# Optimization experiments

Measured on AMD Instinct MI355X. Metric: run time of the kernel, lower is better.

## Reference

```python
import jax, jax.numpy as jnp
import numpy as np

SOS = 1
H = 1024   # hidden_size
V = 32000  # vocab_size
B = 64     # batch
S = 50     # encoder (source) length
T = 25     # decode steps (target length)


def setup_inputs() -> dict:
    key = jax.random.key(0)
    ks = jax.random.split(key, 16)
    s = 1.0 / np.sqrt(H)

    def u(k, shape):
        return jax.random.uniform(k, shape, jnp.float32, -s, s)

    return {
        "encoder_outputs": jax.random.normal(ks[0], (B, S, H), jnp.float32),
        "encoder_hidden": jax.random.normal(ks[1], (1, B, H), jnp.float32),
        "target_tensor": jax.random.randint(ks[2], (B, T), 0, V),
        "emb": jax.random.normal(ks[3], (V, H), jnp.float32),       # nn.Embedding
        "Wa": u(ks[4], (H, H)), "ba": u(ks[5], (H,)),               # attention query proj
        "Ua": u(ks[6], (H, H)), "bu": u(ks[7], (H,)),               # attention key proj
        "Va": u(ks[8], (H, 1)), "bv": u(ks[9], (1,)),               # attention score vector
        "W_ih": u(ks[10], (3 * H, 2 * H)), "b_ih": u(ks[11], (3 * H,)),  # GRU input weights
        "W_hh": u(ks[12], (3 * H, H)), "b_hh": u(ks[13], (3 * H,)),     # GRU hidden weights
        "Wout": u(ks[14], (V, H)), "bout": u(ks[15], (V,)),         # output linear
    }


def reference(encoder_outputs, encoder_hidden, target_tensor, emb,
              Wa, ba, Ua, bu, Va, bv, W_ih, b_ih, W_hh, b_hh, Wout, bout):
    # Bahdanau key projection is independent of the decode step: precompute once.
    keys_proj = encoder_outputs @ Ua.T + bu        # [B, S, H]
    h0 = encoder_hidden[0]                         # [B, H]

    # Teacher forcing: input at step i is SOS then target[:, :-1]. (Dropout in eval mode = identity.)
    sos = jnp.full((B, 1), SOS, dtype=target_tensor.dtype)
    tokens = jnp.concatenate([sos, target_tensor[:, :-1]], axis=1).T  # [T, B]

    def step(h, tok):
        x_emb = emb[tok]                                         # [B, H]
        q = h @ Wa.T + ba                                        # [B, H] (query = hidden)
        scores = jnp.tanh(q[:, None, :] + keys_proj) @ Va        # [B, S, 1]
        w = jax.nn.softmax(scores[..., 0] + bv[0], axis=-1)      # [B, S]
        context = jnp.einsum('bs,bsh->bh', w, encoder_outputs)   # [B, H]
        x = jnp.concatenate([x_emb, context], axis=-1)           # [B, 2H]
        gx = x @ W_ih.T + b_ih                                   # [B, 3H]
        gh = h @ W_hh.T + b_hh                                   # [B, 3H]
        rx, zx, nx = jnp.split(gx, 3, axis=-1)                   # PyTorch gate order r,z,n
        rh, zh, nh = jnp.split(gh, 3, axis=-1)
        r = jax.nn.sigmoid(rx + rh)
        z = jax.nn.sigmoid(zx + zh)
        n = jnp.tanh(nx + r * nh)
        h_new = (1.0 - z) * n + z * h
        logits = h_new @ Wout.T + bout                           # [B, V]
        return h_new, logits

    _, logits = jax.lax.scan(step, h0, tokens)                   # [T, B, V]
    return jnp.transpose(logits, (1, 0, 2))                      # [B, T, V]
```

## Files before the change

kernel.cpp:

```cpp
#include <hip/hip_runtime.h>
#include <hip/hip_bf16.h>

#define BB_ 64
#define SS_ 50
#define TT_ 25
#define HH_ 1024
#define VV_ 32000

typedef __bf16 bf16x8 __attribute__((ext_vector_type(8)));
typedef float f32x4 __attribute__((ext_vector_type(4)));
typedef unsigned long long u64;

__device__ __forceinline__ unsigned short f2b(float f) {
  unsigned u = __float_as_uint(f);
  u = (u + 0x7FFFu + ((u >> 16) & 1u)) >> 16;
  return (unsigned short)u;
}
__device__ __forceinline__ float b2f_(unsigned short s) {
  return __uint_as_float((unsigned)s << 16);
}
__device__ __forceinline__ float fast_tanh(float x) {
  float e = __expf(2.f * x);
  return 1.f - 2.f / (e + 1.f);
}
__device__ __forceinline__ float fast_sigmoid(float x) {
  return 1.f / (1.f + __expf(-x));
}
__device__ __forceinline__ void gload16(const void* g, void* l) {
  __builtin_amdgcn_global_load_lds((const __attribute__((address_space(1))) void*)g,
                                   (__attribute__((address_space(3))) void*)l, 16, 0, 0);
}
__device__ __forceinline__ bf16x8 ldb8(const unsigned short* p) {
  return *(const bf16x8*)p;
}

__device__ __forceinline__ void cstf(float* p, float v) {
  __hip_atomic_store(p, v, __ATOMIC_RELAXED, __HIP_MEMORY_SCOPE_AGENT);
}
__device__ __forceinline__ void cst4(unsigned* p, unsigned v) {
  __hip_atomic_store(p, v, __ATOMIC_RELAXED, __HIP_MEMORY_SCOPE_AGENT);
}
__device__ __forceinline__ unsigned cadd(unsigned* p) {
  return __hip_atomic_fetch_add(p, 1u, __ATOMIC_RELAXED, __HIP_MEMORY_SCOPE_AGENT);
}
__device__ __forceinline__ unsigned cldu(const unsigned* p) {
  return __hip_atomic_load(p, __ATOMIC_RELAXED, __HIP_MEMORY_SCOPE_AGENT);
}

#define F_QR   0
#define F_GHR  128
#define F_CTXR 256
#define F_HR   384
#define F_MINI 512

__global__ __launch_bounds__(256) void cvt_bf16(const float* __restrict__ src,
                                                unsigned short* __restrict__ dst, long n) {
  long i = ((long)blockIdx.x * 256 + threadIdx.x) * 4;
  if (i >= n) return;
  float4 v = *(const float4*)(src + i);
  *(ushort4*)(dst + i) = make_ushort4(f2b(v.x), f2b(v.y), f2b(v.z), f2b(v.w));
}

__global__ __launch_bounds__(256) void embed_gather(const int* __restrict__ tgt,
                                                    const float* __restrict__ emb,
                                                    unsigned short* __restrict__ X) {
  long idx = ((long)blockIdx.x * 256 + threadIdx.x) * 4;
  if (idx >= (long)1600 * HH_) return;
  int col = (int)(idx & (HH_ - 1));
  int r = (int)(idx >> 10);
  int t = r % 25;
  int tok = (t == 0) ? 1 : tgt[r - 1];
  float4 v = *(const float4*)(emb + (long)tok * HH_ + col);
  *(ushort4*)(X + idx) = make_ushort4(f2b(v.x), f2b(v.y), f2b(v.z), f2b(v.w));
}

__global__ __launch_bounds__(256) void init_h(const float* __restrict__ eh,
                                              unsigned short* __restrict__ HBROT,
                                              unsigned* __restrict__ cnt) {
  if (blockIdx.x == 0) {
    for (int k = threadIdx.x; k < 4096; k += 256) cnt[k] = 0;
  }
  int i = (blockIdx.x * 256 + threadIdx.x) * 4;
  if (i >= BB_ * HH_) return;
  float4 v = *(const float4*)(eh + i);
  *(ushort4*)(HBROT + i) = make_ushort4(f2b(v.x), f2b(v.y), f2b(v.z), f2b(v.w));
}

__global__ __launch_bounds__(256) void gemm128_bt(
    const unsigned short* __restrict__ A, const unsigned short* __restrict__ W,
    const float* __restrict__ bias, float* __restrict__ out, long ldo,
    int Mtiles, int ldw, int Mvalid) {
  __shared__ __align__(16) unsigned short As[128 * 32];
  __shared__ __align__(16) unsigned short Bs[128 * 32];
  int nwg = gridDim.x;
  int orig = blockIdx.x;
  int xcd = orig & 7, lid = orig >> 3;
  int qq = nwg >> 3, rr = nwg & 7;
  int wgid = (xcd < rr ? xcd * (qq + 1) : rr * (qq + 1) + (xcd - rr) * qq) + lid;
  int m0 = (wgid % Mtiles) * 128;
  int n0 = (wgid / Mtiles) * 128;
  int tid = threadIdx.x;
  int w = tid >> 6, l = tid & 63;
  int srow = tid >> 2, scg = tid & 3;
  int mw = (w & 1) * 64, nw = (w >> 1) * 64;

  const unsigned short* Ag0 = A + (long)(m0 + srow) * 1024 + scg * 8;
  const unsigned short* Ag1 = Ag0 + 64 * 1024;
  const unsigned short* Wg0 = W + (long)(n0 + srow) * ldw + scg * 8;
  const unsigned short* Wg1 = Wg0 + (long)64 * ldw;
  unsigned short* lA0 = As + tid * 8;
  unsigned short* lA1 = As + 2048 + tid * 8;
  unsigned short* lB0 = Bs + tid * 8;
  unsigned short* lB1 = Bs + 2048 + tid * 8;

  f32x4 zero = {0.f, 0.f, 0.f, 0.f};
  f32x4 acc[4][4];
#pragma unroll
  for (int i = 0; i < 4; ++i)
#pragma unroll
    for (int j = 0; j < 4; ++j) acc[i][j] = zero;

  for (int k0 = 0; k0 < 1024; k0 += 32) {
    __syncthreads();
    gload16(Ag0 + k0, lA0);
    gload16(Ag1 + k0, lA1);
    gload16(Wg0 + k0, lB0);
    gload16(Wg1 + k0, lB1);
    __syncthreads();
    bf16x8 af[4], bg[4];
#pragma unroll
    for (int mt = 0; mt < 4; ++mt)
      af[mt] = ldb8(As + (mw + mt * 16 + (l & 15)) * 32 + (l >> 4) * 8);
#pragma unroll
    for (int nt = 0; nt < 4; ++nt)
      bg[nt] = ldb8(Bs + (nw + nt * 16 + (l & 15)) * 32 + (l >> 4) * 8);
#pragma unroll
    for (int mt = 0; mt < 4; ++mt)
#pragma unroll
      for (int nt = 0; nt < 4; ++nt)
        acc[mt][nt] = __builtin_amdgcn_mfma_f32_16x16x32_bf16(af[mt], bg[nt], acc[mt][nt], 0, 0, 0);
  }

  int lr = (l >> 4) * 4, lc = l & 15;
#pragma unroll
  for (int nt = 0; nt < 4; ++nt) {
    int col = n0 + nw + nt * 16 + lc;
    float bv = bias[col];
#pragma unroll
    for (int mt = 0; mt < 4; ++mt) {
#pragma unroll
      for (int r = 0; r < 4; ++r) {
        int m = m0 + mw + mt * 16 + lr + r;
        if (m < Mvalid) out[(long)m * ldo + col] = acc[mt][nt][r] + bv;
      }
    }
  }
}

__global__ __launch_bounds__(256) void decode_loop(
    const unsigned short* __restrict__ WaB, const unsigned short* __restrict__ WhhB,
    const unsigned short* __restrict__ WihB, const float* __restrict__ ba,
    const float* __restrict__ bhh, const float* __restrict__ Va,
    const unsigned short* __restrict__ KEYSB, const unsigned short* __restrict__ ENCB,
    const float* __restrict__ GA, const float* __restrict__ ehid,
    float* __restrict__ QROT, float* __restrict__ GHROT, float* __restrict__ SCROT,
    unsigned short* __restrict__ CTXROT, unsigned short* __restrict__ HBROT,
    unsigned short* __restrict__ HALLB, unsigned* __restrict__ cnt) {
  __shared__ __align__(16) char AsC[16 * 2048];
  __shared__ float qs[1024];
  __shared__ float vas[1024];
  __shared__ float wgt[64];

  const int tid = threadIdx.x, bid = blockIdx.x;
  const int wv = tid >> 6, l = tid & 63;
  const int lc = l & 15, hi = l >> 4, ko = hi * 8, lr4 = hi * 4;
  const int xcd = bid & 7, lxb = bid >> 3;
  const int mt_ = lxb & 3, cg = lxb >> 2;
  const int qcls = xcd >> 1;

  const int m1 = mt_ * 16;
  const int nch = xcd * 32 + cg * 4 + wv;
  const int n1 = nch * 16;
  const bool isq = (n1 < 1024);
  const unsigned short* B1 = isq ? WaB + (long)(n1 + lc) * 1024 + ko
                                 : WhhB + (long)(n1 - 1024 + lc) * 1024 + ko;
  float* o1 = isq ? QROT + n1 : GHROT + (n1 - 1024);
  const long ldo1 = isq ? 1024 : 3072;
  const long slot1 = isq ? (long)BB_ * 1024 : (long)BB_ * 3072;
  const float bv1 = isq ? ba[n1 + lc] : bhh[n1 - 1024 + lc];

  const int b2 = xcd * 8 + cg;
  const int jq = mt_ * 4 + wv;
  const int c2 = mt_ * 256 + tid;

  const int m3 = mt_ * 16, n3 = (xcd * 8 + cg) * 16;
  const unsigned short* Bg0 = WihB + (long)(n3 + lc) * 2048 + 1024 + ko;
  const unsigned short* Bg1 = Bg0 + (long)1024 * 2048;
  const unsigned short* Bg2 = Bg0 + (long)2048 * 2048;
  const int ig = n3 + lc;
  float hreg[4];
  if (tid < 64) {
#pragma unroll
    for (int r = 0; r < 4; ++r) hreg[r] = ehid[(long)(m3 + lr4 + r) * HH_ + ig];
  }

#pragma unroll
  for (int j = 0; j < 4; ++j) vas[tid + j * 256] = Va[tid + j * 256];

  const f32x4 zero = {0.f, 0.f, 0.f, 0.f};

  for (int t = 0; t < TT_; ++t) {
    if (tid == 0) {
      while (cldu(cnt + F_HR + mt_ * 32) < (unsigned)t * 64u) __builtin_amdgcn_s_sleep(4);
    }
    __syncthreads();

    {
      const unsigned short* hbase = HBROT + (long)t * (BB_ * 1024);
#pragma unroll
      for (int i = 0; i < 16; ++i) {
        u64 v = *((const u64*)(hbase + (long)(m1 + i) * 1024) + tid);
        *(u64*)(AsC + ((i * 2048 + tid * 8) ^ ((i & 7) << 4))) = v;
      }
      __syncthreads();
      f32x4 acc = zero;
#pragma unroll 8
      for (int k = 0; k < 1024; k += 32) {
        bf16x8 af = *(const bf16x8*)(AsC + ((lc * 2048 + (k + ko) * 2) ^ ((lc & 7) << 4)));
        acc = __builtin_amdgcn_mfma_f32_16x16x32_bf16(af, ldb8(B1 + k), acc, 0, 0, 0);
      }
#pragma unroll
      for (int r = 0; r < 4; ++r)
        cstf(o1 + (long)t * slot1 + (long)(m1 + lr4 + r) * ldo1 + lc, acc[r] + bv1);
    }
    __syncthreads();
    if (tid == 0) {
      cadd(cnt + (isq ? F_QR : F_GHR) + mt_ * 32);
      while (cldu(cnt + F_QR + qcls * 32) < (unsigned)(t + 1) * 16u) __builtin_amdgcn_s_sleep(4);
    }
    __syncthreads();

    {
      const float* qsl = QROT + (long)t * (BB_ * 1024) + (long)b2 * 1024;
#pragma unroll
      for (int j = 0; j < 4; ++j)
        qs[tid + j * 256] = qsl[tid + j * 256];
      __syncthreads();
      for (int s = jq; s < SS_; s += 16) {
        const unsigned short* kr = KEYSB + ((long)b2 * SS_ + s) * 1024;
        float p = 0.f;
#pragma unroll
        for (int j = 0; j < 16; ++j) {
          int hh = l + j * 64;
          p += fast_tanh(qs[hh] + b2f_(kr[hh])) * vas[hh];
        }
#pragma unroll
        for (int off = 32; off; off >>= 1) p += __shfl_down(p, off);
        if (l == 0) cstf(SCROT + (long)t * 4096 + b2 * 64 + s, p);
      }
    }
    __syncthreads();
    if (tid == 0) {
      unsigned* mc = cnt + F_MINI + b2 * 32;
      cadd(mc);
      while (cldu(mc) < (unsigned)(t + 1) * 4u) __builtin_amdgcn_s_sleep(4);
    }
    __syncthreads();

    {
      if (tid < 64) {
        float v = (tid < SS_) ? SCROT[(long)t * 4096 + b2 * 64 + tid] : -1e30f;
        float m = v;
#pragma unroll
        for (int off = 32; off; off >>= 1) m = fmaxf(m, __shfl_down(m, off));
        m = __shfl(m, 0);
        float e = (tid < SS_) ? __expf(v - m) : 0.f;
        float ssum = e;
#pragma unroll
        for (int off = 32; off; off >>= 1) ssum += __shfl_down(ssum, off);
        ssum = __shfl(ssum, 0);
        if (tid < SS_) wgt[tid] = e / ssum;
      }
      __syncthreads();
      {
        const unsigned short* ep = ENCB + (long)b2 * SS_ * 1024 + c2;
        float a0 = 0.f;
#pragma unroll 10
        for (int s = 0; s < SS_; ++s)
          a0 += wgt[s] * b2f_(ep[(long)s * 1024]);
        unsigned hb16 = (unsigned)f2b(a0);
        unsigned ob = (unsigned)__shfl_xor((int)hb16, 1);
        if ((tid & 1) == 0)
          cst4((unsigned*)(CTXROT + (long)t * (BB_ * 1024) + (long)b2 * 1024 + c2), hb16 | (ob << 16));
      }
    }
    __syncthreads();
    if (tid == 0) {
      cadd(cnt + F_CTXR + qcls * 32);
      while (cldu(cnt + F_CTXR + mt_ * 32) < (unsigned)(t + 1) * 64u) __builtin_amdgcn_s_sleep(4);
      while (cldu(cnt + F_GHR + mt_ * 32) < (unsigned)(t + 1) * 48u) __builtin_amdgcn_s_sleep(4);
    }
    __syncthreads();

    {
      const unsigned short* cbase = CTXROT + (long)t * (BB_ * 1024);
#pragma unroll
      for (int i = 0; i < 16; ++i) {
        u64 v = *((const u64*)(cbase + (long)(m3 + i) * 1024) + tid);
        *(u64*)(AsC + ((i * 2048 + tid * 8) ^ ((i & 7) << 4))) = v;
      }
      __syncthreads();
      if (tid < 64) {
        f32x4 ar = zero, az = zero, an_ = zero;
#pragma unroll 8
        for (int k = 0; k < 1024; k += 32) {
          bf16x8 a = *(const bf16x8*)(AsC + ((lc * 2048 + (k + ko) * 2) ^ ((lc & 7) << 4)));
          ar = __builtin_amdgcn_mfma_f32_16x16x32_bf16(a, ldb8(Bg0 + k), ar, 0, 0, 0);
          az = __builtin_amdgcn_mfma_f32_16x16x32_bf16(a, ldb8(Bg1 + k), az, 0, 0, 0);
          an_ = __builtin_amdgcn_mfma_f32_16x16x32_bf16(a, ldb8(Bg2 + k), an_, 0, 0, 0);
        }
        const float* ghb = GHROT + (long)t * (BB_ * 3072);
        unsigned short* hnb = HBROT + (long)(t + 1) * (BB_ * 1024);
#pragma unroll
        for (int r = 0; r < 4; ++r) {
          int bb = m3 + lr4 + r;
          long rowBT = (long)bb * TT_ + t;
          const float* ga = GA + rowBT * 3072;
          const float* gh = ghb + (long)bb * 3072;
          float rr = fast_sigmoid(ga[ig] + ar[r] + gh[ig]);
          float zz = fast_sigmoid(ga[1024 + ig] + az[r] + gh[1024 + ig]);
          float nn = fast_tanh(ga[2048 + ig] + an_[r] + rr * gh[2048 + ig]);
          float hnew = (1.f - zz) * nn + zz * hreg[r];
          hreg[r] = hnew;
          unsigned hb = (unsigned)f2b(hnew);
          unsigned ob = (unsigned)__shfl_xor((int)hb, 1);
          if ((lc & 1) == 0)
            cst4((unsigned*)(hnb + (long)bb * 1024 + ig), hb | (ob << 16));
          HALLB[rowBT * HH_ + ig] = (unsigned short)hb;
        }
      }
    }
    __syncthreads();
    if (tid == 0) cadd(cnt + F_HR + mt_ * 32);
  }
}

extern "C" void kernel_launch(void* const* d_in, const int* in_sizes, int n_in,
                              void* d_out, int out_size, void* d_ws, size_t ws_size,
                              hipStream_t stream) {
  (void)in_sizes; (void)n_in; (void)out_size; (void)ws_size;
  const float* enc  = (const float*)d_in[0];
  const float* ehid = (const float*)d_in[1];
  const int*   tgt  = (const int*)d_in[2];
  const float* emb  = (const float*)d_in[3];
  const float* Wa   = (const float*)d_in[4];
  const float* ba   = (const float*)d_in[5];
  const float* Ua   = (const float*)d_in[6];
  const float* bu   = (const float*)d_in[7];
  const float* Va   = (const float*)d_in[8];
  const float* Wih  = (const float*)d_in[10];
  const float* bih  = (const float*)d_in[11];
  const float* Whh  = (const float*)d_in[12];
  const float* bhh  = (const float*)d_in[13];
  const float* Wout = (const float*)d_in[14];
  const float* bout = (const float*)d_in[15];
  float* out = (float*)d_out;

  char* p = (char*)d_ws;
  auto alloc = [&](size_t bytes) { char* r = p; p += (bytes + 255) & ~(size_t)255; return r; };
  unsigned short* WOUTB = (unsigned short*)alloc((size_t)VV_ * HH_ * 2);
  unsigned short* WIHB  = (unsigned short*)alloc((size_t)3072 * 2048 * 2);
  unsigned short* WHHB  = (unsigned short*)alloc((size_t)3072 * 1024 * 2);
  unsigned short* WAB   = (unsigned short*)alloc((size_t)1024 * 1024 * 2);
  unsigned short* UAB   = (unsigned short*)alloc((size_t)1024 * 1024 * 2);
  unsigned short* ENCB  = (unsigned short*)alloc((size_t)BB_ * SS_ * HH_ * 2);
  unsigned short* XEMB  = (unsigned short*)alloc((size_t)1664 * HH_ * 2);
  unsigned short* HALLB = (unsigned short*)alloc((size_t)1664 * HH_ * 2);
  float* KEYS = (float*)alloc((size_t)BB_ * SS_ * HH_ * 4);
  unsigned short* KEYSB = (unsigned short*)alloc((size_t)BB_ * SS_ * HH_ * 2);
  float* GA   = (float*)alloc((size_t)1600 * 3072 * 4);
  float* QROT  = (float*)alloc((size_t)TT_ * BB_ * 1024 * 4);
  float* GHROT = (float*)alloc((size_t)TT_ * BB_ * 3072 * 4);
  float* SCROT = (float*)alloc((size_t)TT_ * 4096 * 4);
  unsigned short* CTXROT = (unsigned short*)alloc((size_t)TT_ * BB_ * 1024 * 2);
  unsigned short* HBROT  = (unsigned short*)alloc((size_t)(TT_ + 1) * BB_ * 1024 * 2);
  unsigned* CNT = (unsigned*)alloc(4096 * 4);

  auto cvt = [&](const float* s, unsigned short* d, long n) {
    cvt_bf16<<<dim3((unsigned)((n / 4 + 255) / 256)), dim3(256), 0, stream>>>(s, d, n);
  };
  cvt(Wout, WOUTB, (long)VV_ * HH_);
  cvt(Wih, WIHB, (long)3072 * 2048);
  cvt(Whh, WHHB, (long)3072 * 1024);
  cvt(Wa, WAB, (long)1024 * 1024);
  cvt(Ua, UAB, (long)1024 * 1024);
  cvt(enc, ENCB, (long)BB_ * SS_ * HH_);
  embed_gather<<<dim3(1600 * HH_ / 4 / 256), dim3(256), 0, stream>>>(tgt, emb, XEMB);
  init_h<<<dim3(BB_ * HH_ / 4 / 256), dim3(256), 0, stream>>>(ehid, HBROT, CNT);

  gemm128_bt<<<dim3(25 * 8), dim3(256), 0, stream>>>(ENCB, UAB, bu, KEYS, (long)1024, 25, 1024, 3200);
  cvt(KEYS, KEYSB, (long)BB_ * SS_ * HH_);
  gemm128_bt<<<dim3(13 * 24), dim3(256), 0, stream>>>(XEMB, WIHB, bih, GA, (long)3072, 13, 2048, 1600);

  decode_loop<<<dim3(256), dim3(256), 0, stream>>>(
      WAB, WHHB, WIHB, ba, bhh, Va, KEYSB, ENCB, GA, ehid,
      QROT, GHROT, SCROT, CTXROT, HBROT, HALLB, CNT);

  gemm128_bt<<<dim3(13 * 250), dim3(256), 0, stream>>>(HALLB, WOUTB, bout, out, (long)VV_, 13, 1024, 1600);
}
```

Measured before the change: 1.660 ms.

## Replace atomic counter barriers with per-producer epoch flags polled in parallel

```diff
diff --git a/kernel.cpp b/kernel.cpp
--- a/kernel.cpp
+++ b/kernel.cpp
@@ -40,18 +40,16 @@
 __device__ __forceinline__ void cst4(unsigned* p, unsigned v) {
   __hip_atomic_store(p, v, __ATOMIC_RELAXED, __HIP_MEMORY_SCOPE_AGENT);
 }
-__device__ __forceinline__ unsigned cadd(unsigned* p) {
-  return __hip_atomic_fetch_add(p, 1u, __ATOMIC_RELAXED, __HIP_MEMORY_SCOPE_AGENT);
-}
 __device__ __forceinline__ unsigned cldu(const unsigned* p) {
   return __hip_atomic_load(p, __ATOMIC_RELAXED, __HIP_MEMORY_SCOPE_AGENT);
 }
 
-#define F_QR   0
-#define F_GHR  128
-#define F_CTXR 256
-#define F_HR   384
-#define F_MINI 512
+#define W_HR(c, j)   (cnt + ((c) * 64 + (j)) * 32)
+#define W_CTX(c, j)  (cnt + (256 + (c) * 64 + (j)) * 32)
+#define W_QR(c, p)   (cnt + (512 + (c) * 16 + (p)) * 32)
+#define W_GH(c, p)   (cnt + (576 + (c) * 48 + (p)) * 32)
+#define W_MINI(b, k) (cnt + (768 + (b) * 4 + (k)) * 32)
+#define CNT_DWORDS 32768
 
 __global__ __launch_bounds__(256) void cvt_bf16(const float* __restrict__ src,
                                                 unsigned short* __restrict__ dst, long n) {
@@ -78,7 +76,7 @@
                                               unsigned short* __restrict__ HBROT,
                                               unsigned* __restrict__ cnt) {
   if (blockIdx.x == 0) {
-    for (int k = threadIdx.x; k < 4096; k += 256) cnt[k] = 0;
+    for (int k = threadIdx.x; k < CNT_DWORDS; k += 256) cnt[k] = 0;
   }
   int i = (blockIdx.x * 256 + threadIdx.x) * 4;
   if (i >= BB_ * HH_) return;
@@ -178,6 +176,11 @@
   const int mt_ = lxb & 3, cg = lxb >> 2;
   const int qcls = xcd >> 1;
 
+  const int hidx = xcd * 8 + cg;
+  const int cidx = (xcd & 1) * 32 + lxb;
+  const int qidx = (xcd & 1) * 8 + cg;
+  const int gidx = (xcd - 2) * 8 + cg;
+
   const int m1 = mt_ * 16;
   const int nch = xcd * 32 + cg * 4 + wv;
   const int n1 = nch * 16;
@@ -210,8 +213,10 @@
   const f32x4 zero = {0.f, 0.f, 0.f, 0.f};
 
   for (int t = 0; t < TT_; ++t) {
-    if (tid == 0) {
-      while (cldu(cnt + F_HR + mt_ * 32) < (unsigned)t * 64u) __builtin_amdgcn_s_sleep(4);
+    const unsigned ep = (unsigned)(t + 1);
+    if (tid < 64) {
+      const unsigned* w = W_HR(mt_, tid);
+      while (cldu(w) < (unsigned)t) __builtin_amdgcn_s_sleep(1);
     }
     __syncthreads();
 
@@ -234,9 +239,10 @@
         cstf(o1 + (long)t * slot1 + (long)(m1 + lr4 + r) * ldo1 + lc, acc[r] + bv1);
     }
     __syncthreads();
-    if (tid == 0) {
-      cadd(cnt + (isq ? F_QR : F_GHR) + mt_ * 32);
-      while (cldu(cnt + F_QR + qcls * 32) < (unsigned)(t + 1) * 16u) __builtin_amdgcn_s_sleep(4);
+    if (tid == 0) cst4(isq ? W_QR(mt_, qidx) : W_GH(mt_, gidx), ep);
+    if (tid < 16) {
+      const unsigned* w = W_QR(qcls, tid);
+      while (cldu(w) < ep) __builtin_amdgcn_s_sleep(1);
     }
     __syncthreads();
 
@@ -260,10 +266,10 @@
       }
     }
     __syncthreads();
-    if (tid == 0) {
-      unsigned* mc = cnt + F_MINI + b2 * 32;
-      cadd(mc);
-      while (cldu(mc) < (unsigned)(t + 1) * 4u) __builtin_amdgcn_s_sleep(4);
+    if (tid == 0) cst4(W_MINI(b2, mt_), ep);
+    if (tid < 4) {
+      const unsigned* w = W_MINI(b2, tid);
+      while (cldu(w) < ep) __builtin_amdgcn_s_sleep(1);
     }
     __syncthreads();
 
@@ -283,11 +289,11 @@
       }
       __syncthreads();
       {
-        const unsigned short* ep = ENCB + (long)b2 * SS_ * 1024 + c2;
+        const unsigned short* ep_ = ENCB + (long)b2 * SS_ * 1024 + c2;
         float a0 = 0.f;
 #pragma unroll 10
         for (int s = 0; s < SS_; ++s)
-          a0 += wgt[s] * b2f_(ep[(long)s * 1024]);
+          a0 += wgt[s] * b2f_(ep_[(long)s * 1024]);
         unsigned hb16 = (unsigned)f2b(a0);
         unsigned ob = (unsigned)__shfl_xor((int)hb16, 1);
         if ((tid & 1) == 0)
@@ -295,10 +301,13 @@
       }
     }
     __syncthreads();
-    if (tid == 0) {
-      cadd(cnt + F_CTXR + qcls * 32);
-      while (cldu(cnt + F_CTXR + mt_ * 32) < (unsigned)(t + 1) * 64u) __builtin_amdgcn_s_sleep(4);
-      while (cldu(cnt + F_GHR + mt_ * 32) < (unsigned)(t + 1) * 48u) __builtin_amdgcn_s_sleep(4);
+    if (tid == 0) cst4(W_CTX(qcls, cidx), ep);
+    if (tid < 64) {
+      const unsigned* w = W_CTX(mt_, tid);
+      while (cldu(w) < ep) __builtin_amdgcn_s_sleep(1);
+    } else if (tid < 112) {
+      const unsigned* w = W_GH(mt_, tid - 64);
+      while (cldu(w) < ep) __builtin_amdgcn_s_sleep(1);
     }
     __syncthreads();
 
@@ -341,7 +350,7 @@
       }
     }
     __syncthreads();
-    if (tid == 0) cadd(cnt + F_HR + mt_ * 32);
+    if (tid == 0) cst4(W_HR(mt_, hidx), ep);
   }
 }
 
@@ -384,7 +393,7 @@
   float* SCROT = (float*)alloc((size_t)TT_ * 4096 * 4);
   unsigned short* CTXROT = (unsigned short*)alloc((size_t)TT_ * BB_ * 1024 * 2);
   unsigned short* HBROT  = (unsigned short*)alloc((size_t)(TT_ + 1) * BB_ * 1024 * 2);
-  unsigned* CNT = (unsigned*)alloc(4096 * 4);
+  unsigned* CNT = (unsigned*)alloc((size_t)CNT_DWORDS * 4);
 
   auto cvt = [&](const float* s, unsigned short* d, long n) {
     cvt_bf16<<<dim3((unsigned)((n / 4 + 255) / 256)), dim3(256), 0, stream>>>(s, d, n);
```

Result: no change. 1.666 ms (+0.4%).
